# Kernel tuning notes

Measured on AMD Instinct MI355X. Metric: run time of the kernel, lower is better.

## Reference

```python
import jax, jax.numpy as jnp
import numpy as np

CHANNELS = 512
COND_DIM = 768
NUM_HEADS = 8
NUM_GROUPS = 32
EPS = 1e-5


def setup_inputs() -> dict:
    key = jax.random.key(0)
    ks = jax.random.split(key, 8)
    B, H, W, C, S = 8, 64, 64, CHANNELS, 256
    x = jax.random.normal(ks[0], (B, H, W, C), dtype=jnp.float32)
    cond_tokens = jax.random.normal(ks[1], (B, S, COND_DIM), dtype=jnp.float32)
    gn_scale = jnp.ones((C,), dtype=jnp.float32)
    gn_bias = jnp.zeros((C,), dtype=jnp.float32)
    Wq = jax.random.normal(ks[2], (C, CHANNELS), dtype=jnp.float32) * 0.02
    Wk = jax.random.normal(ks[3], (COND_DIM, CHANNELS), dtype=jnp.float32) * 0.02
    Wv = jax.random.normal(ks[4], (COND_DIM, CHANNELS), dtype=jnp.float32) * 0.02
    Wo = jax.random.normal(ks[5], (CHANNELS, CHANNELS), dtype=jnp.float32) * 0.02
    bo = jnp.zeros((CHANNELS,), dtype=jnp.float32)
    return {"x": x, "cond_tokens": cond_tokens, "gn_scale": gn_scale,
            "gn_bias": gn_bias, "Wq": Wq, "Wk": Wk, "Wv": Wv, "Wo": Wo, "bo": bo}


def group_norm(x, scale, bias):
    # x: (B,H,W,C); normalize over H,W and channels within each of NUM_GROUPS groups
    b, h, w, c = x.shape
    xg = x.reshape(b, h, w, NUM_GROUPS, c // NUM_GROUPS)
    mean = jnp.mean(xg, axis=(1, 2, 4), keepdims=True)
    var = jnp.var(xg, axis=(1, 2, 4), keepdims=True)
    xn = (xg - mean) * jax.lax.rsqrt(var + EPS)
    return xn.reshape(b, h, w, c) * scale + bias


def reference(x, cond_tokens, gn_scale, gn_bias, Wq, Wk, Wv, Wo, bo):
    b, h, w, c = x.shape
    head_dim = CHANNELS // NUM_HEADS
    x_seq = group_norm(x, gn_scale, gn_bias).reshape(b, h * w, c)
    # projections
    q = (x_seq @ Wq).reshape(b, -1, NUM_HEADS, head_dim).transpose(0, 2, 1, 3)
    k = (cond_tokens @ Wk).reshape(b, -1, NUM_HEADS, head_dim).transpose(0, 2, 1, 3)
    v = (cond_tokens @ Wv).reshape(b, -1, NUM_HEADS, head_dim).transpose(0, 2, 1, 3)
    scores = jnp.einsum('bhqd,bhkd->bhqk', q, k) / np.sqrt(head_dim).astype(np.float32)
    attn = jax.nn.softmax(scores, axis=-1)
    out = jnp.einsum('bhqk,bhkd->bhqd', attn, v)
    out = out.transpose(0, 2, 1, 3).reshape(b, h * w, CHANNELS)
    out = out @ Wo + bo
    return x + out.reshape(b, h, w, c)
```

## Files before the change

### kernel.cpp

```cpp
#include <hip/hip_runtime.h>
#include <hip/hip_bf16.h>

typedef unsigned short u16;
typedef unsigned int u32;
typedef __attribute__((ext_vector_type(8))) __bf16 bf16x8;
typedef __attribute__((ext_vector_type(4))) float f32x4;
typedef __attribute__((ext_vector_type(16))) float f32x16;
typedef __attribute__((ext_vector_type(4))) u32 u32x4;

#define DEVFN static __device__ __forceinline__

DEVFN float bf2f(u16 v) { union { u32 u; float f; } x; x.u = (u32)v << 16; return x.f; }
DEVFN u16 f2bf(float f) {
    union { float f; u32 u; } x; x.f = f;
    u32 r = x.u + 0x7fff + ((x.u >> 16) & 1);
    return (u16)(r >> 16);
}

union BF2 { struct { __bf16 lo, hi; } s; u32 w; };
DEVFN u32 pk2(float a, float b) { BF2 t; t.s.lo = (__bf16)a; t.s.hi = (__bf16)b; return t.w; }

DEVFN void gload_lds16(const u16* g, u16* l) {
    __builtin_amdgcn_global_load_lds((const __attribute__((address_space(1))) u32*)g,
                                     (__attribute__((address_space(3))) u32*)l, 16, 0, 0);
}

template<int BN, int OUTMODE, bool BIAS, bool RES>
__global__ __launch_bounds__(256)
void gemm_bt(const u16* __restrict__ A, const u16* __restrict__ B,
             void* __restrict__ Cv, const float* __restrict__ bias,
             const float* __restrict__ res,
             int K, int lda, int ldb, int ldc,
             long sAb, long sAh, long sBb, long sBh, long sCb, long sCh,
             float scale)
{
    constexpr int NF = BN / 32;
    __shared__ u16 smem[4096 + BN * 32];
    const int tid = threadIdx.x;
    const int lane = tid & 63, wave = tid >> 6;
    const int wr = wave >> 1, wc = wave & 1;
    const int z = blockIdx.z, zb = z >> 3, zh = z & 7;

    const u16* Ab = A + zb * sAb + zh * sAh + (long)blockIdx.x * 128 * lda;
    const u16* Bb = B + zb * sBb + zh * sBh + (long)blockIdx.y * BN * ldb;

    const int ra = tid >> 2, ca = (tid & 3) * 8;
    const u16* pA0 = Ab + (long)ra * lda + ca;
    const u16* pA1 = Ab + (long)(ra + 64) * lda + ca;
    u16* lA0 = smem + tid * 8;
    u16* lA1 = smem + (256 + tid) * 8;
    const u16* pB0 = Bb + (long)ra * ldb + ca;
    const u16* pB1 = Bb + (long)(ra + 64) * ldb + ca;
    u16* lB0 = smem + 4096 + tid * 8;
    u16* lB1 = smem + 4096 + (256 + tid) * 8;

    const int foff = ((lane & 15) * 4 + (lane >> 4)) * 8;
    const u16* aF = smem + wr * 2048 + foff;
    const u16* bF = smem + 4096 + wc * (NF * 512) + foff;

    f32x4 acc[4][NF];
#pragma unroll
    for (int i = 0; i < 4; ++i)
#pragma unroll
        for (int j = 0; j < NF; ++j) acc[i][j] = (f32x4){0.f, 0.f, 0.f, 0.f};

    for (int k0 = 0; k0 < K; k0 += 32) {
        gload_lds16(pA0 + k0, lA0);
        gload_lds16(pA1 + k0, lA1);
        gload_lds16(pB0 + k0, lB0);
        if constexpr (BN == 128) gload_lds16(pB1 + k0, lB1);
        asm volatile("s_waitcnt vmcnt(0)" ::: "memory");
        __syncthreads();
        bf16x8 av[4], bv[NF];
#pragma unroll
        for (int i = 0; i < 4; ++i) av[i] = *(const bf16x8*)(aF + i * 512);
#pragma unroll
        for (int j = 0; j < NF; ++j) bv[j] = *(const bf16x8*)(bF + j * 512);
#pragma unroll
        for (int i = 0; i < 4; ++i)
#pragma unroll
            for (int j = 0; j < NF; ++j)
                acc[i][j] = __builtin_amdgcn_mfma_f32_16x16x32_bf16(av[i], bv[j], acc[i][j], 0, 0, 0);
        __syncthreads();
    }

    const int m0 = blockIdx.x * 128 + wr * 64 + (lane >> 4) * 4;
    const int n0 = blockIdx.y * BN + wc * (BN / 2) + (lane & 15);
    if constexpr (OUTMODE == 0) {
        u16* Cb = (u16*)Cv + zb * sCb + zh * sCh;
#pragma unroll
        for (int i = 0; i < 4; ++i)
#pragma unroll
            for (int j = 0; j < NF; ++j) {
                int n = n0 + j * 16;
#pragma unroll
                for (int r = 0; r < 4; ++r) {
                    int m = m0 + i * 16 + r;
                    Cb[(long)m * ldc + n] = f2bf(acc[i][j][r] * scale);
                }
            }
    } else if constexpr (OUTMODE == 1) {
        float* Cb = (float*)Cv + zb * sCb + zh * sCh;
#pragma unroll
        for (int i = 0; i < 4; ++i)
#pragma unroll
            for (int j = 0; j < NF; ++j) {
                int n = n0 + j * 16;
                float bv_ = BIAS ? bias[n] : 0.f;
#pragma unroll
                for (int r = 0; r < 4; ++r) {
                    int m = m0 + i * 16 + r;
                    float v = acc[i][j][r] * scale + bv_;
                    if constexpr (RES) v += res[(long)m * ldc + n];
                    Cb[(long)m * ldc + n] = v;
                }
            }
    } else {
#pragma unroll
        for (int i = 0; i < 4; ++i) {
            int m = m0 + i * 16;
            int b = m >> 8, s = m & 255;
#pragma unroll
            for (int j = 0; j < NF; ++j) {
                int n = n0 + j * 16;
                int h = n >> 6, d = n & 63;
                ushort4 pk;
                pk.x = f2bf(acc[i][j][0]); pk.y = f2bf(acc[i][j][1]);
                pk.z = f2bf(acc[i][j][2]); pk.w = f2bf(acc[i][j][3]);
                *(ushort4*)((u16*)Cv + (((long)(b * 8 + h) * 64 + d) * 256 + s)) = pk;
            }
        }
    }
}

union U8 { u32 w[4]; bf16x8 v; };

__global__ __launch_bounds__(512, 4)
void attn_fused(const u16* __restrict__ Q, const u16* __restrict__ K,
                const u16* __restrict__ Vt, u16* __restrict__ O)
{
    __shared__ u16 lds[40960];
    const int tid = threadIdx.x, lane = tid & 63, wave = tid >> 6;
    const int bh = blockIdx.y, b = bh >> 3, h = bh & 7;
    const int l31 = lane & 31, lh = lane >> 5;
    const long q0 = (long)b * 4096 + blockIdx.x * 256 + wave * 32;
    const bool hiHalf = (lh != 0);

    {
        const u16* Kb_ = K + (long)b * 256 * 512 + h * 64;
        const u16* Vb_ = Vt + (long)bh * 16384;
#pragma unroll
        for (int it = 0; it < 4; ++it) {
            int f = it * 8 + wave;
            int st = f >> 2, kc = f & 3;
            gload_lds16(Kb_ + (long)(st * 32 + l31) * 512 + kc * 16 + lh * 8,
                        lds + f * 512 + lane * 8);
            int dt = f >> 4, ks = f & 15;
            gload_lds16(Vb_ + (long)(dt * 32 + l31) * 256 + ks * 16 + lh * 8,
                        lds + 16384 + f * 512 + lane * 8);
        }
    }
    bf16x8 qf[4];
    {
        const u16* Qp = Q + (q0 + l31) * 512 + h * 64 + lh * 8;
#pragma unroll
        for (int kc = 0; kc < 4; ++kc) qf[kc] = *(const bf16x8*)(Qp + kc * 16);
    }
    asm volatile("s_waitcnt vmcnt(0)" ::: "memory");
    __syncthreads();

    f32x16 oacc[2];
#pragma unroll
    for (int dt = 0; dt < 2; ++dt)
#pragma unroll
        for (int r = 0; r < 16; ++r) oacc[dt][r] = 0.f;
    float m_run = -3e38f, sum_run = 0.f;

#pragma unroll
    for (int st = 0; st < 8; ++st) {
        f32x16 sc;
#pragma unroll
        for (int r = 0; r < 16; ++r) sc[r] = 0.f;
        __builtin_amdgcn_s_setprio(1);
#pragma unroll
        for (int kc = 0; kc < 4; ++kc) {
            bf16x8 af = *(const bf16x8*)(lds + (st * 4 + kc) * 512 + lane * 8);
            sc = __builtin_amdgcn_mfma_f32_32x32x16_bf16(af, qf[kc], sc, 0, 0, 0);
        }
        __builtin_amdgcn_s_setprio(0);
        float tm = sc[0];
#pragma unroll
        for (int r = 1; r < 16; ++r) tm = fmaxf(tm, sc[r]);
        tm = fmaxf(tm, __shfl_xor(tm, 32));
        if (!__all(tm <= m_run + 8.f)) {
            float mnew = fmaxf(m_run, tm);
            float fac = exp2f(m_run - mnew);
            m_run = mnew;
            sum_run *= fac;
#pragma unroll
            for (int dt = 0; dt < 2; ++dt)
#pragma unroll
                for (int r = 0; r < 16; ++r) oacc[dt][r] *= fac;
        }
#pragma unroll
        for (int r = 0; r < 16; ++r) {
            float e = exp2f(sc[r] - m_run);
            sc[r] = e; sum_run += e;
        }
        u32 c[8], x[8];
#pragma unroll
        for (int i = 0; i < 8; ++i) c[i] = pk2(sc[2 * i], sc[2 * i + 1]);
#pragma unroll
        for (int i = 0; i < 8; ++i) x[i] = (u32)__shfl_xor((int)c[i], 32);
        U8 p0, p1;
        p0.w[0] = hiHalf ? x[2] : c[0];  p0.w[1] = hiHalf ? x[3] : c[1];
        p0.w[2] = hiHalf ? c[2] : x[0];  p0.w[3] = hiHalf ? c[3] : x[1];
        p1.w[0] = hiHalf ? x[6] : c[4];  p1.w[1] = hiHalf ? x[7] : c[5];
        p1.w[2] = hiHalf ? c[6] : x[4];  p1.w[3] = hiHalf ? c[7] : x[5];
        __builtin_amdgcn_s_setprio(1);
#pragma unroll
        for (int dt = 0; dt < 2; ++dt) {
            bf16x8 v0 = *(const bf16x8*)(lds + 16384 + (dt * 16 + st * 2) * 512 + lane * 8);
            bf16x8 v1 = *(const bf16x8*)(lds + 16384 + (dt * 16 + st * 2 + 1) * 512 + lane * 8);
            oacc[dt] = __builtin_amdgcn_mfma_f32_32x32x16_bf16(v0, p0.v, oacc[dt], 0, 0, 0);
            oacc[dt] = __builtin_amdgcn_mfma_f32_32x32x16_bf16(v1, p1.v, oacc[dt], 0, 0, 0);
        }
        __builtin_amdgcn_s_setprio(0);
    }

    sum_run += __shfl_xor(sum_run, 32);
    float inv = 1.f / sum_run;

    u16* ow = lds + 32768 + (wave & 3) * 2048;
    const int shift = wave >> 2;
#pragma unroll
    for (int s_ = 0; s_ < 2; ++s_) {
        if (s_ == 1) __syncthreads();
        if (shift == s_) {
            const int q = l31;
#pragma unroll
            for (int dt = 0; dt < 2; ++dt)
#pragma unroll
                for (int rq = 0; rq < 4; ++rq) {
                    int d = dt * 32 + rq * 8 + 4 * lh;
                    u32 w0 = pk2(oacc[dt][rq * 4 + 0] * inv, oacc[dt][rq * 4 + 1] * inv);
                    u32 w1 = pk2(oacc[dt][rq * 4 + 2] * inv, oacc[dt][rq * 4 + 3] * inv);
                    int byte = q * 128 + ((d * 2) ^ ((q & 7) << 4));
                    *(u32*)((char*)ow + byte) = w0;
                    *(u32*)((char*)ow + byte + 4) = w1;
                }
#pragma unroll
            for (int i = 0; i < 4; ++i) {
                int qq = (lane >> 3) + i * 8;
                int byte = qq * 128 + (((lane & 7) * 16) ^ ((qq & 7) << 4));
                bf16x8 val = *(const bf16x8*)((char*)ow + byte);
                *(bf16x8*)(O + (q0 + qq) * 512 + h * 64 + (lane & 7) * 8) = val;
            }
        }
    }
}

__global__ __launch_bounds__(256)
void gn_stats(const float* __restrict__ x, const float* __restrict__ gscale,
              const float* __restrict__ gbias, float* __restrict__ coefA,
              float* __restrict__ coefD)
{
    const int b = blockIdx.x >> 5, g = blockIdx.x & 31;
    const float* base = x + (long)b * 4096 * 512 + g * 16;
    const int tid = threadIdx.x;
    const int p0 = tid >> 2, c0 = (tid & 3) * 4;
    const float* tp = base + (long)p0 * 512 + c0;
    float sum = 0.f, sq = 0.f;
    for (int it = 0; it < 64; ++it) {
        float4 v = *(const float4*)(tp + (long)it * 64 * 512);
        sum += v.x + v.y + v.z + v.w;
        sq += v.x * v.x + v.y * v.y + v.z * v.z + v.w * v.w;
    }
#pragma unroll
    for (int off = 32; off; off >>= 1) {
        sum += __shfl_down(sum, off);
        sq  += __shfl_down(sq, off);
    }
    __shared__ float ssum[4], ssq[4];
    if ((tid & 63) == 0) { ssum[tid >> 6] = sum; ssq[tid >> 6] = sq; }
    __syncthreads();
    if (tid < 16) {
        float S = ssum[0] + ssum[1] + ssum[2] + ssum[3];
        float Q = ssq[0] + ssq[1] + ssq[2] + ssq[3];
        float mean = S * (1.f / 65536.f);
        float var = Q * (1.f / 65536.f) - mean * mean;
        float rstd = rsqrtf(var + 1e-5f);
        int c = g * 16 + tid;
        float a = gscale[c] * rstd;
        coefA[b * 512 + c] = a;
        coefD[b * 512 + c] = gbias[c] - mean * a;
    }
}

__global__ __launch_bounds__(256)
void gn_apply(const float* __restrict__ x, const float* __restrict__ coefA,
              const float* __restrict__ coefD, u16* __restrict__ xn, int nvec)
{
    for (long v8 = blockIdx.x * 256 + threadIdx.x; v8 < nvec; v8 += (long)gridDim.x * 256) {
        long e = v8 * 8;
        int b = (int)(e >> 21);
        int c = (int)(e & 511);
        float4 v0 = *(const float4*)(x + e);
        float4 v1 = *(const float4*)(x + e + 4);
        const float* pa = coefA + b * 512 + c;
        const float* pd = coefD + b * 512 + c;
        float f[8] = { v0.x, v0.y, v0.z, v0.w, v1.x, v1.y, v1.z, v1.w };
        u32x4 o;
#pragma unroll
        for (int q = 0; q < 4; ++q) {
            float g0 = f[q * 2] * pa[q * 2] + pd[q * 2];
            float g1 = f[q * 2 + 1] * pa[q * 2 + 1] + pd[q * 2 + 1];
            o[q] = (u32)f2bf(g0) | ((u32)f2bf(g1) << 16);
        }
        *(u32x4*)(xn + e) = o;
    }
}

__global__ __launch_bounds__(256)
void conv_bf16(const float* __restrict__ in, u16* __restrict__ out)
{
    long e = ((long)blockIdx.x * 256 + threadIdx.x) * 8;
    float4 v0 = *(const float4*)(in + e);
    float4 v1 = *(const float4*)(in + e + 4);
    float f[8] = { v0.x, v0.y, v0.z, v0.w, v1.x, v1.y, v1.z, v1.w };
    u32x4 o;
#pragma unroll
    for (int q = 0; q < 4; ++q)
        o[q] = (u32)f2bf(f[q * 2]) | ((u32)f2bf(f[q * 2 + 1]) << 16);
    *(u32x4*)(out + e) = o;
}

__global__ __launch_bounds__(256)
void transpose_all(const float* __restrict__ Wq, const float* __restrict__ Wk,
                   const float* __restrict__ Wv, const float* __restrict__ Wo,
                   u16* __restrict__ WqT, u16* __restrict__ WkT,
                   u16* __restrict__ WvT, u16* __restrict__ WoT)
{
    __shared__ u16 t[32][33];
    const int z = blockIdx.z;
    const float* in = (z == 0) ? Wq : (z == 1) ? Wk : (z == 2) ? Wv : Wo;
    u16* out = (z == 0) ? WqT : (z == 1) ? WkT : (z == 2) ? WvT : WoT;
    const int R = (z == 1 || z == 2) ? 768 : 512, C = 512;
    const int r0 = blockIdx.y * 32, c0 = blockIdx.x * 32;
    if (r0 >= R) return;
    int tx = threadIdx.x & 31, ty = threadIdx.x >> 5;
    for (int i = ty; i < 32; i += 8) t[i][tx] = f2bf(in[(long)(r0 + i) * C + c0 + tx]);
    __syncthreads();
    for (int i = ty; i < 32; i += 8) out[(long)(c0 + i) * R + r0 + tx] = t[tx][i];
}

extern "C" void kernel_launch(void* const* d_in, const int* in_sizes, int n_in,
                              void* d_out, int out_size, void* d_ws, size_t ws_size,
                              hipStream_t stream)
{
    const float* x    = (const float*)d_in[0];
    const float* cond = (const float*)d_in[1];
    const float* gsc  = (const float*)d_in[2];
    const float* gbi  = (const float*)d_in[3];
    const float* Wq   = (const float*)d_in[4];
    const float* Wk   = (const float*)d_in[5];
    const float* Wv   = (const float*)d_in[6];
    const float* Wo   = (const float*)d_in[7];
    const float* bo   = (const float*)d_in[8];

    char* ws = (char*)d_ws;
    size_t off = 0;
    auto alloc = [&](size_t bytes) -> void* {
        void* p = ws + off; off += (bytes + 255) & ~(size_t)255; return p;
    };
    u16* WqT   = (u16*)alloc(512 * 512 * 2);
    u16* WkT   = (u16*)alloc(512 * 768 * 2);
    u16* WvT   = (u16*)alloc(512 * 768 * 2);
    u16* WoT   = (u16*)alloc(512 * 512 * 2);
    float* cfA = (float*)alloc(8 * 512 * 4);
    float* cfD = (float*)alloc(8 * 512 * 4);
    u16* condb = (u16*)alloc(2048l * 768 * 2);
    u16* xn    = (u16*)alloc(33554432);
    u16* Qb    = (u16*)alloc(33554432);
    u16* Kb    = (u16*)alloc(2048l * 512 * 2);
    u16* Vt    = (u16*)alloc(2097152);
    u16* Ob = xn;

    transpose_all<<<dim3(16, 24, 4), 256, 0, stream>>>(Wq, Wk, Wv, Wo, WqT, WkT, WvT, WoT);
    conv_bf16<<<768, 256, 0, stream>>>(cond, condb);

    gn_stats<<<256, 256, 0, stream>>>(x, gsc, gbi, cfA, cfD);
    gn_apply<<<2048, 256, 0, stream>>>(x, cfA, cfD, xn, 2097152);

    gemm_bt<128, 0, false, false><<<dim3(256, 4, 1), 256, 0, stream>>>(
        xn, WqT, Qb, nullptr, nullptr, 512, 512, 512, 512,
        0, 0, 0, 0, 0, 0, 0.18033688011112042f);
    gemm_bt<128, 0, false, false><<<dim3(16, 4, 1), 256, 0, stream>>>(
        condb, WkT, Kb, nullptr, nullptr, 768, 768, 768, 512,
        0, 0, 0, 0, 0, 0, 1.f);
    gemm_bt<128, 2, false, false><<<dim3(16, 4, 1), 256, 0, stream>>>(
        condb, WvT, Vt, nullptr, nullptr, 768, 768, 768, 0,
        0, 0, 0, 0, 0, 0, 1.f);

    attn_fused<<<dim3(16, 64), 512, 0, stream>>>(Qb, Kb, Vt, Ob);

    gemm_bt<128, 1, true, true><<<dim3(256, 4, 1), 256, 0, stream>>>(
        Ob, WoT, d_out, bo, x, 512, 512, 512, 512,
        0, 0, 0, 0, 0, 0, 1.f);
}
```

Measured before the change: 200.0 us.

## Fuse GroupNorm apply into Q GEMM, split stats, widen K-step, stage epilogue

Removes the separate gn_apply pass. The Q projection GEMM now loads fp32 x directly, applies the per-channel GroupNorm affine coefficients and converts to bf16 into LDS. GroupNorm statistics are split into a wide partial-sum kernel over row chunks and a small coefficient kernel, which gives more parallelism than one block per group. The GEMM K-step doubles to 64, and the fp32 output epilogue goes through LDS so stores and residual reads are coalesced float4. The cost is that the Q GEMM's A loads become synchronous register loads instead of async LDS loads, and it reads 4x the bytes of x, since fp32 x is read once per N-tile.

```diff
diff --git a/kernel.cpp b/kernel.cpp
--- a/kernel.cpp
+++ b/kernel.cpp
@@ -25,73 +25,97 @@
                                      (__attribute__((address_space(3))) u32*)l, 16, 0, 0);
 }
 
-template<int BN, int OUTMODE, bool BIAS, bool RES>
+template<int OUTMODE, bool BIAS, bool RES, bool AFF>
 __global__ __launch_bounds__(256)
-void gemm_bt(const u16* __restrict__ A, const u16* __restrict__ B,
+void gemm_bt(const void* __restrict__ Av, const u16* __restrict__ B,
              void* __restrict__ Cv, const float* __restrict__ bias,
              const float* __restrict__ res,
-             int K, int lda, int ldb, int ldc,
-             long sAb, long sAh, long sBb, long sBh, long sCb, long sCh,
-             float scale)
-{
-    constexpr int NF = BN / 32;
-    __shared__ u16 smem[4096 + BN * 32];
+             const float* __restrict__ cfA, const float* __restrict__ cfD,
+             int K, int lda, int ldb, int ldc, float scale)
+{
+    __shared__ u16 smem[16384];
     const int tid = threadIdx.x;
     const int lane = tid & 63, wave = tid >> 6;
     const int wr = wave >> 1, wc = wave & 1;
-    const int z = blockIdx.z, zb = z >> 3, zh = z & 7;
-
-    const u16* Ab = A + zb * sAb + zh * sAh + (long)blockIdx.x * 128 * lda;
-    const u16* Bb = B + zb * sBb + zh * sBh + (long)blockIdx.y * BN * ldb;
-
-    const int ra = tid >> 2, ca = (tid & 3) * 8;
-    const u16* pA0 = Ab + (long)ra * lda + ca;
-    const u16* pA1 = Ab + (long)(ra + 64) * lda + ca;
-    u16* lA0 = smem + tid * 8;
-    u16* lA1 = smem + (256 + tid) * 8;
-    const u16* pB0 = Bb + (long)ra * ldb + ca;
-    const u16* pB1 = Bb + (long)(ra + 64) * ldb + ca;
-    u16* lB0 = smem + 4096 + tid * 8;
-    u16* lB1 = smem + 4096 + (256 + tid) * 8;
-
+
+    const u16* Bb = B + (long)blockIdx.y * 128 * ldb;
     const int foff = ((lane & 15) * 4 + (lane >> 4)) * 8;
-    const u16* aF = smem + wr * 2048 + foff;
-    const u16* bF = smem + 4096 + wc * (NF * 512) + foff;
-
-    f32x4 acc[4][NF];
+
+    f32x4 acc[4][4];
 #pragma unroll
     for (int i = 0; i < 4; ++i)
 #pragma unroll
-        for (int j = 0; j < NF; ++j) acc[i][j] = (f32x4){0.f, 0.f, 0.f, 0.f};
-
-    for (int k0 = 0; k0 < K; k0 += 32) {
-        gload_lds16(pA0 + k0, lA0);
-        gload_lds16(pA1 + k0, lA1);
-        gload_lds16(pB0 + k0, lB0);
-        if constexpr (BN == 128) gload_lds16(pB1 + k0, lB1);
+        for (int j = 0; j < 4; ++j) acc[i][j] = (f32x4){0.f, 0.f, 0.f, 0.f};
+
+    for (int k0 = 0; k0 < K; k0 += 64) {
+#pragma unroll
+        for (int p = 0; p < 4; ++p) {
+            int row = ((p & 1) * 4 + (tid >> 6)) * 16 + ((tid & 63) >> 2);
+            int chl = (p >> 1) * 32 + (tid & 3) * 8;
+            gload_lds16(Bb + (long)row * ldb + k0 + chl,
+                        smem + 8192 + (p * 256 + tid) * 8);
+        }
+        if constexpr (AFF) {
+            const float* xf = (const float*)Av;
+#pragma unroll
+            for (int p = 0; p < 4; ++p) {
+                int row = ((p & 1) * 4 + (tid >> 6)) * 16 + ((tid & 63) >> 2);
+                int chl = (p >> 1) * 32 + (tid & 3) * 8;
+                long m = (long)blockIdx.x * 128 + row;
+                int c = k0 + chl;
+                const float* src = xf + m * lda + c;
+                float4 v0 = *(const float4*)(src);
+                float4 v1 = *(const float4*)(src + 4);
+                int cb = (int)((m >> 12) << 9) + c;
+                float4 a0 = *(const float4*)(cfA + cb);
+                float4 a1 = *(const float4*)(cfA + cb + 4);
+                float4 d0 = *(const float4*)(cfD + cb);
+                float4 d1 = *(const float4*)(cfD + cb + 4);
+                u32x4 o;
+                o[0] = pk2(v0.x * a0.x + d0.x, v0.y * a0.y + d0.y);
+                o[1] = pk2(v0.z * a0.z + d0.z, v0.w * a0.w + d0.w);
+                o[2] = pk2(v1.x * a1.x + d1.x, v1.y * a1.y + d1.y);
+                o[3] = pk2(v1.z * a1.z + d1.z, v1.w * a1.w + d1.w);
+                *(u32x4*)(smem + (p * 256 + tid) * 8) = o;
+            }
+        } else {
+            const u16* Ab = (const u16*)Av + (long)blockIdx.x * 128 * lda;
+#pragma unroll
+            for (int p = 0; p < 4; ++p) {
+                int row = ((p & 1) * 4 + (tid >> 6)) * 16 + ((tid & 63) >> 2);
+                int chl = (p >> 1) * 32 + (tid & 3) * 8;
+                gload_lds16(Ab + (long)row * lda + k0 + chl,
+                            smem + (p * 256 + tid) * 8);
+            }
+        }
         asm volatile("s_waitcnt vmcnt(0)" ::: "memory");
         __syncthreads();
-        bf16x8 av[4], bv[NF];
-#pragma unroll
-        for (int i = 0; i < 4; ++i) av[i] = *(const bf16x8*)(aF + i * 512);
-#pragma unroll
-        for (int j = 0; j < NF; ++j) bv[j] = *(const bf16x8*)(bF + j * 512);
+#pragma unroll
+        for (int kk = 0; kk < 2; ++kk) {
+            bf16x8 av[4], bv[4];
+#pragma unroll
+            for (int i = 0; i < 4; ++i)
+                av[i] = *(const bf16x8*)(smem + kk * 4096 + (wr * 4 + i) * 512 + foff);
+#pragma unroll
+            for (int j = 0; j < 4; ++j)
+                bv[j] = *(const bf16x8*)(smem + 8192 + kk * 4096 + (wc * 4 + j) * 512 + foff);
+#pragma unroll
+            for (int i = 0; i < 4; ++i)
+#pragma unroll
+                for (int j = 0; j < 4; ++j)
+                    acc[i][j] = __builtin_amdgcn_mfma_f32_16x16x32_bf16(av[i], bv[j], acc[i][j], 0, 0, 0);
+        }
+        __syncthreads();
+    }
+
+    const int m0 = blockIdx.x * 128 + wr * 64 + (lane >> 4) * 4;
+    const int n0 = blockIdx.y * 128 + wc * 64 + (lane & 15);
+    if constexpr (OUTMODE == 0) {
+        u16* Cb = (u16*)Cv;
 #pragma unroll
         for (int i = 0; i < 4; ++i)
 #pragma unroll
-            for (int j = 0; j < NF; ++j)
-                acc[i][j] = __builtin_amdgcn_mfma_f32_16x16x32_bf16(av[i], bv[j], acc[i][j], 0, 0, 0);
-        __syncthreads();
-    }
-
-    const int m0 = blockIdx.x * 128 + wr * 64 + (lane >> 4) * 4;
-    const int n0 = blockIdx.y * BN + wc * (BN / 2) + (lane & 15);
-    if constexpr (OUTMODE == 0) {
-        u16* Cb = (u16*)Cv + zb * sCb + zh * sCh;
-#pragma unroll
-        for (int i = 0; i < 4; ++i)
-#pragma unroll
-            for (int j = 0; j < NF; ++j) {
+            for (int j = 0; j < 4; ++j) {
                 int n = n0 + j * 16;
 #pragma unroll
                 for (int r = 0; r < 4; ++r) {
@@ -100,28 +124,48 @@
                 }
             }
     } else if constexpr (OUTMODE == 1) {
-        float* Cb = (float*)Cv + zb * sCb + zh * sCh;
-#pragma unroll
-        for (int i = 0; i < 4; ++i)
-#pragma unroll
-            for (int j = 0; j < NF; ++j) {
-                int n = n0 + j * 16;
-                float bv_ = BIAS ? bias[n] : 0.f;
+        float* cl = (float*)smem;
+        float* Co = (float*)Cv;
+#pragma unroll
+        for (int i = 0; i < 4; ++i) {
+            __syncthreads();
+#pragma unroll
+            for (int j = 0; j < 4; ++j)
 #pragma unroll
                 for (int r = 0; r < 4; ++r) {
-                    int m = m0 + i * 16 + r;
-                    float v = acc[i][j][r] * scale + bv_;
-                    if constexpr (RES) v += res[(long)m * ldc + n];
-                    Cb[(long)m * ldc + n] = v;
+                    int rl = wr * 16 + (lane >> 4) * 4 + r;
+                    int col = wc * 64 + j * 16 + (lane & 15);
+                    cl[rl * 132 + col] = acc[i][j][r];
                 }
-            }
+            __syncthreads();
+            int rl = tid >> 3;
+            int c0 = (tid & 7) * 16;
+            long m = (long)blockIdx.x * 128 + i * 16 + (rl & 15) + (rl >> 4) * 64;
+            long n = (long)blockIdx.y * 128 + c0;
+#pragma unroll
+            for (int q = 0; q < 4; ++q) {
+                float4 v = *(float4*)(cl + rl * 132 + c0 + q * 4);
+                float4 o;
+                o.x = v.x * scale; o.y = v.y * scale;
+                o.z = v.z * scale; o.w = v.w * scale;
+                if constexpr (BIAS) {
+                    float4 b4 = *(const float4*)(bias + n + q * 4);
+                    o.x += b4.x; o.y += b4.y; o.z += b4.z; o.w += b4.w;
+                }
+                if constexpr (RES) {
+                    float4 r4 = *(const float4*)(res + m * ldc + n + q * 4);
+                    o.x += r4.x; o.y += r4.y; o.z += r4.z; o.w += r4.w;
+                }
+                *(float4*)(Co + m * ldc + n + q * 4) = o;
+            }
+        }
     } else {
 #pragma unroll
         for (int i = 0; i < 4; ++i) {
             int m = m0 + i * 16;
             int b = m >> 8, s = m & 255;
 #pragma unroll
-            for (int j = 0; j < NF; ++j) {
+            for (int j = 0; j < 4; ++j) {
                 int n = n0 + j * 16;
                 int h = n >> 6, d = n & 63;
                 ushort4 pk;
@@ -261,63 +305,54 @@
 }
 
 __global__ __launch_bounds__(256)
-void gn_stats(const float* __restrict__ x, const float* __restrict__ gscale,
-              const float* __restrict__ gbias, float* __restrict__ coefA,
-              float* __restrict__ coefD)
-{
-    const int b = blockIdx.x >> 5, g = blockIdx.x & 31;
-    const float* base = x + (long)b * 4096 * 512 + g * 16;
-    const int tid = threadIdx.x;
-    const int p0 = tid >> 2, c0 = (tid & 3) * 4;
-    const float* tp = base + (long)p0 * 512 + c0;
+void gn_part(const float* __restrict__ x, float* __restrict__ part)
+{
+    const int b = blockIdx.x, ch = blockIdx.y;
+    const float* base = x + ((long)b * 4096 + ch * 64) * 512;
+    const int t = threadIdx.x;
+    const int c4 = t & 127, r0 = t >> 7;
     float sum = 0.f, sq = 0.f;
-    for (int it = 0; it < 64; ++it) {
-        float4 v = *(const float4*)(tp + (long)it * 64 * 512);
+    for (int rr = r0; rr < 64; rr += 2) {
+        float4 v = *(const float4*)(base + (long)rr * 512 + c4 * 4);
         sum += v.x + v.y + v.z + v.w;
-        sq += v.x * v.x + v.y * v.y + v.z * v.z + v.w * v.w;
-    }
-#pragma unroll
-    for (int off = 32; off; off >>= 1) {
-        sum += __shfl_down(sum, off);
-        sq  += __shfl_down(sq, off);
-    }
-    __shared__ float ssum[4], ssq[4];
-    if ((tid & 63) == 0) { ssum[tid >> 6] = sum; ssq[tid >> 6] = sq; }
+        sq  += v.x * v.x + v.y * v.y + v.z * v.z + v.w * v.w;
+    }
+    __shared__ float s0[128], s1[128];
+    if (t >= 128) { s0[c4] = sum; s1[c4] = sq; }
     __syncthreads();
-    if (tid < 16) {
-        float S = ssum[0] + ssum[1] + ssum[2] + ssum[3];
-        float Q = ssq[0] + ssq[1] + ssq[2] + ssq[3];
-        float mean = S * (1.f / 65536.f);
-        float var = Q * (1.f / 65536.f) - mean * mean;
-        float rstd = rsqrtf(var + 1e-5f);
-        int c = g * 16 + tid;
+    if (t < 128) {
+        sum += s0[c4]; sq += s1[c4];
+        sum += __shfl_down(sum, 2); sum += __shfl_down(sum, 1);
+        sq  += __shfl_down(sq, 2);  sq  += __shfl_down(sq, 1);
+        if ((t & 3) == 0) {
+            int g = t >> 2;
+            float* pp = part + (long)(b * 64 + ch) * 64;
+            pp[g] = sum; pp[32 + g] = sq;
+        }
+    }
+}
+
+__global__ __launch_bounds__(256)
+void gn_coef(const float* __restrict__ part, const float* __restrict__ gscale,
+             const float* __restrict__ gbias, float* __restrict__ coefA,
+             float* __restrict__ coefD)
+{
+    const int t = threadIdx.x;
+    const int b = t >> 5, g = t & 31;
+    float S = 0.f, Q = 0.f;
+    for (int ch = 0; ch < 64; ++ch) {
+        const float* pp = part + (long)(b * 64 + ch) * 64;
+        S += pp[g]; Q += pp[32 + g];
+    }
+    float mean = S * (1.f / 65536.f);
+    float var = Q * (1.f / 65536.f) - mean * mean;
+    float rstd = rsqrtf(var + 1e-5f);
+#pragma unroll
+    for (int cc = 0; cc < 16; ++cc) {
+        int c = g * 16 + cc;
         float a = gscale[c] * rstd;
         coefA[b * 512 + c] = a;
         coefD[b * 512 + c] = gbias[c] - mean * a;
-    }
-}
-
-__global__ __launch_bounds__(256)
-void gn_apply(const float* __restrict__ x, const float* __restrict__ coefA,
-              const float* __restrict__ coefD, u16* __restrict__ xn, int nvec)
-{
-    for (long v8 = blockIdx.x * 256 + threadIdx.x; v8 < nvec; v8 += (long)gridDim.x * 256) {
-        long e = v8 * 8;
-        int b = (int)(e >> 21);
-        int c = (int)(e & 511);
-        float4 v0 = *(const float4*)(x + e);
-        float4 v1 = *(const float4*)(x + e + 4);
-        const float* pa = coefA + b * 512 + c;
-        const float* pd = coefD + b * 512 + c;
-        float f[8] = { v0.x, v0.y, v0.z, v0.w, v1.x, v1.y, v1.z, v1.w };
-        u32x4 o;
-#pragma unroll
-        for (int q = 0; q < 4; ++q) {
-            float g0 = f[q * 2] * pa[q * 2] + pd[q * 2];
-            float g1 = f[q * 2 + 1] * pa[q * 2 + 1] + pd[q * 2 + 1];
-            o[q] = (u32)f2bf(g0) | ((u32)f2bf(g1) << 16);
-        }
-        *(u32x4*)(xn + e) = o;
     }
 }
 
@@ -373,38 +408,35 @@
     auto alloc = [&](size_t bytes) -> void* {
         void* p = ws + off; off += (bytes + 255) & ~(size_t)255; return p;
     };
-    u16* WqT   = (u16*)alloc(512 * 512 * 2);
-    u16* WkT   = (u16*)alloc(512 * 768 * 2);
-    u16* WvT   = (u16*)alloc(512 * 768 * 2);
-    u16* WoT   = (u16*)alloc(512 * 512 * 2);
-    float* cfA = (float*)alloc(8 * 512 * 4);
-    float* cfD = (float*)alloc(8 * 512 * 4);
-    u16* condb = (u16*)alloc(2048l * 768 * 2);
-    u16* xn    = (u16*)alloc(33554432);
-    u16* Qb    = (u16*)alloc(33554432);
-    u16* Kb    = (u16*)alloc(2048l * 512 * 2);
-    u16* Vt    = (u16*)alloc(2097152);
-    u16* Ob = xn;
+    u16* WqT    = (u16*)alloc(512 * 512 * 2);
+    u16* WkT    = (u16*)alloc(512 * 768 * 2);
+    u16* WvT    = (u16*)alloc(512 * 768 * 2);
+    u16* WoT    = (u16*)alloc(512 * 512 * 2);
+    float* cfA  = (float*)alloc(8 * 512 * 4);
+    float* cfD  = (float*)alloc(8 * 512 * 4);
+    float* part = (float*)alloc(8 * 64 * 64 * 4);
+    u16* condb  = (u16*)alloc(2048l * 768 * 2);
+    u16* Ob     = (u16*)alloc(33554432);
+    u16* Qb     = (u16*)alloc(33554432);
+    u16* Kb     = (u16*)alloc(2048l * 512 * 2);
+    u16* Vt     = (u16*)alloc(2097152);
 
     transpose_all<<<dim3(16, 24, 4), 256, 0, stream>>>(Wq, Wk, Wv, Wo, WqT, WkT, WvT, WoT);
     conv_bf16<<<768, 256, 0, stream>>>(cond, condb);
 
-    gn_stats<<<256, 256, 0, stream>>>(x, gsc, gbi, cfA, cfD);
-    gn_apply<<<2048, 256, 0, stream>>>(x, cfA, cfD, xn, 2097152);
-
-    gemm_bt<128, 0, false, false><<<dim3(256, 4, 1), 256, 0, stream>>>(
-        xn, WqT, Qb, nullptr, nullptr, 512, 512, 512, 512,
-        0, 0, 0, 0, 0, 0, 0.18033688011112042f);
-    gemm_bt<128, 0, false, false><<<dim3(16, 4, 1), 256, 0, stream>>>(
-        condb, WkT, Kb, nullptr, nullptr, 768, 768, 768, 512,
-        0, 0, 0, 0, 0, 0, 1.f);
-    gemm_bt<128, 2, false, false><<<dim3(16, 4, 1), 256, 0, stream>>>(
-        condb, WvT, Vt, nullptr, nullptr, 768, 768, 768, 0,
-        0, 0, 0, 0, 0, 0, 1.f);
+    gn_part<<<dim3(8, 64), 256, 0, stream>>>(x, part);
+    gn_coef<<<1, 256, 0, stream>>>(part, gsc, gbi, cfA, cfD);
+
+    gemm_bt<0, false, false, true><<<dim3(256, 4), 256, 0, stream>>>(
+        x, WqT, Qb, nullptr, nullptr, cfA, cfD, 512, 512, 512, 512,
+        0.18033688011112042f);
+    gemm_bt<0, false, false, false><<<dim3(16, 4), 256, 0, stream>>>(
+        condb, WkT, Kb, nullptr, nullptr, nullptr, nullptr, 768, 768, 768, 512, 1.f);
+    gemm_bt<2, false, false, false><<<dim3(16, 4), 256, 0, stream>>>(
+        condb, WvT, Vt, nullptr, nullptr, nullptr, nullptr, 768, 768, 768, 0, 1.f);
 
     attn_fused<<<dim3(16, 64), 512, 0, stream>>>(Qb, Kb, Vt, Ob);
 
-    gemm_bt<128, 1, true, true><<<dim3(256, 4, 1), 256, 0, stream>>>(
-        Ob, WoT, d_out, bo, x, 512, 512, 512, 512,
-        0, 0, 0, 0, 0, 0, 1.f);
-}
+    gemm_bt<1, true, true, false><<<dim3(256, 4), 256, 0, stream>>>(
+        Ob, WoT, d_out, bo, x, nullptr, nullptr, 512, 512, 512, 512, 1.f);
+}
```

Result: faster. 195.4 us (-2.3%).
